# Kernel tuning notes

Measured on AMD Instinct MI355X. Metric: run time of the kernel, lower is better.

Reference implementation:

```python
import jax, jax.numpy as jnp
from jax import lax
import numpy as np

D_IN, D, H, W, POOL = 1280, 100, 20, 3, 9
K_SIG, X0 = 1.0, 0.0
EPS = 1e-5


def setup_inputs() -> dict:
    key = jax.random.key(0)
    ks = jax.random.split(key, 8)
    N1, N2 = 512, 512
    return {
        "x1": jax.random.normal(ks[0], (N1, D_IN), jnp.float32),
        "x2": jax.random.normal(ks[1], (N2, D_IN), jnp.float32),
        "W1": jax.random.normal(ks[2], (D, D_IN), jnp.float32) * 0.02,
        "b1": jnp.zeros((D,), jnp.float32),
        "W2": jax.random.normal(ks[3], (H, 2 * D), jnp.float32) * 0.05,
        "b2": jnp.zeros((H,), jnp.float32),
        "bn1_g": jnp.ones((H,), jnp.float32),
        "bn1_b": jnp.zeros((H,), jnp.float32),
        "conv_w": jax.random.normal(ks[4], (1, H, 2 * W + 1, 2 * W + 1), jnp.float32) * 0.05,
        "conv_b": jnp.zeros((1,), jnp.float32),
        "bn2_g": jnp.ones((1,), jnp.float32),
        "bn2_b": jnp.zeros((1,), jnp.float32),
        "gamma": jnp.zeros((1,), jnp.float32),
    }


def reference(x1, x2, W1, b1, W2, b2, bn1_g, bn1_b, conv_w, conv_b, bn2_g, bn2_b, gamma):
    N1, N2 = x1.shape[0], x2.shape[0]
    # fc1 projection (relu1/dropout1 are defined but unused in the original forward)
    a = (x1 @ W1.T + b1)[None]          # [1, N1, D]
    c = (x2 @ W1.T + b2 * 0 + b1)[None] if False else (x2 @ W1.T + b1)[None]  # [1, N2, D]
    # broadcast pairwise |diff| and product -> [1, N1, N2, 2D]
    diff = jnp.abs(a[:, :, None, :] - c[:, None, :, :])
    mul = a[:, :, None, :] * c[:, None, :, :]
    m = jnp.concatenate([diff, mul], axis=-1).reshape(-1, 2 * D)  # [N1*N2, 2D]
    # fc2
    m = m @ W2.T + b2                    # [N1*N2, H]
    # BatchNorm1d in training mode: batch statistics, biased variance
    mu = m.mean(axis=0)
    var = m.var(axis=0)
    m = (m - mu) * lax.rsqrt(var + EPS) * bn1_g + bn1_b
    m = jax.nn.relu(m)
    m = m.reshape(1, N1, N2, H).transpose(0, 3, 1, 2)  # NCHW [1, H, N1, N2]
    # 7x7 conv, padding=W
    C = lax.conv_general_dilated(m, conv_w, (1, 1), [(W, W), (W, W)])
    C = C + conv_b.reshape(1, -1, 1, 1)
    # BatchNorm2d (training mode, biased variance over N,H,W per channel)
    mu2 = C.mean(axis=(0, 2, 3), keepdims=True)
    var2 = C.var(axis=(0, 2, 3), keepdims=True)
    C = (C - mu2) * lax.rsqrt(var2 + EPS) * bn2_g.reshape(1, -1, 1, 1) + bn2_b.reshape(1, -1, 1, 1)
    C = jax.nn.sigmoid(C)
    # MaxPool2d(9, padding=4): stride = kernel, -inf padding
    p = POOL // 2
    B = lax.reduce_window(C, -jnp.inf, lax.max, (1, 1, POOL, POOL), (1, 1, POOL, POOL),
                          [(0, 0), (0, 0), (p, p), (p, p)])
    # mean / unbiased std over dims (1, 2) keepdim
    mean = B.mean(axis=(1, 2), keepdims=True)
    std = jnp.sqrt(B.var(axis=(1, 2), keepdims=True, ddof=1) + EPS)
    Q = jax.nn.relu(B - mean - gamma.reshape(()) * std)
    phat = Q.sum() / (jnp.sign(Q).sum() + 1.0)
    phat = jnp.clip(jax.nn.sigmoid(K_SIG * (phat - X0)), 0.0, 1.0)
    return phat, C
```

## Files before the change

### kernel.cpp

```cpp
#include <hip/hip_runtime.h>
#include <hip/hip_bf16.h>
#include <math.h>

#define N1 512
#define N2 512
#define DIN 1280
#define DD 100
#define HH 20
#define NPIX (N1*N2)
#define PB 57

typedef short bf16x8 __attribute__((ext_vector_type(8)));
typedef float f32x4 __attribute__((ext_vector_type(4)));

static constexpr size_t WS_PP    = 0;
static constexpr size_t WS_W1T   = 409600;
static constexpr size_t WS_W2B   = 537600;
static constexpr size_t WS_M     = 541696;
static constexpr size_t WS_PART  = WS_M + 5242880;
static constexpr size_t WS_CRAW  = WS_PART + 1310720;
static constexpr size_t WS_STATS = WS_CRAW + 262144;
static constexpr size_t WS_B     = WS_STATS + 64;

__global__ __launch_bounds__(256) void kP(const float* __restrict__ W1,
                                          const float* __restrict__ W2,
                                          float* __restrict__ w1t,
                                          unsigned short* __restrict__ w2b,
                                          float* __restrict__ stats) {
  const int tid = threadIdx.x;
  if (blockIdx.x >= 160) {
    int idx = (blockIdx.x - 160) * 256 + tid;
    if (blockIdx.x == 160 && tid < 64) stats[tid] = 0.0f;
    if (idx < 224 * 32) {
      int k = idx >> 5, n = idx & 31;
      float v = (n < HH && k < 200) ? W2[n * 200 + k] : 0.0f;
      __hip_bfloat16 b = __float2bfloat16(v);
      w2b[idx] = *reinterpret_cast<unsigned short*>(&b);
    }
    return;
  }
  __shared__ float sT[32][33];
  const int bx = blockIdx.x % 40, by = blockIdx.x / 40;
  const int tx = tid & 31, ty = tid >> 5;
#pragma unroll
  for (int e = 0; e < 4; ++e) {
    int h = by * 32 + ty + e * 8, k = bx * 32 + tx;
    sT[ty + e * 8][tx] = (h < DD) ? W1[(size_t)h * DIN + k] : 0.0f;
  }
  __syncthreads();
#pragma unroll
  for (int e = 0; e < 4; ++e) {
    int k = bx * 32 + ty + e * 8, h = by * 32 + tx;
    if (h < DD) w1t[(size_t)k * DD + h] = sT[tx][ty + e * 8];
  }
}

__global__ __launch_bounds__(256) void kA(const float* __restrict__ x1,
                                          const float* __restrict__ x2,
                                          const float* __restrict__ w1t,
                                          float* __restrict__ pp) {
  const int tid = threadIdx.x;
  const int w  = __builtin_amdgcn_readfirstlane(tid >> 6);
  const int rp = w >> 1, hh = w & 1;
  const int h = hh * 64 + (tid & 63);
  if (h >= DD) return;
  const int kq = blockIdx.x & 3;
  const int r0 = (blockIdx.x >> 2) * 4 + rp * 2;
  const float* xb = (r0 < N1) ? (x1 + (size_t)r0 * DIN) : (x2 + (size_t)(r0 - N1) * DIN);
  const float* xr0 = xb + kq * 320;
  const float* xr1 = xb + DIN + kq * 320;
  const float* w1p = w1t + (size_t)kq * 320 * DD + h;
  float a00 = 0.f, a01 = 0.f, a10 = 0.f, a11 = 0.f;
#pragma unroll 8
  for (int k = 0; k < 320; k += 2) {
    float wA = w1p[(size_t)k * DD];
    float wB = w1p[(size_t)(k + 1) * DD];
    a00 = fmaf(wA, xr0[k], a00); a01 = fmaf(wB, xr0[k + 1], a01);
    a10 = fmaf(wA, xr1[k], a10); a11 = fmaf(wB, xr1[k + 1], a11);
  }
  pp[(size_t)kq * 102400 + (size_t)r0 * DD + h] = a00 + a01;
  pp[(size_t)kq * 102400 + (size_t)(r0 + 1) * DD + h] = a10 + a11;
}

__global__ __launch_bounds__(256, 2) void kB(const float* __restrict__ pp,
                                             const float* __restrict__ b1,
                                             const unsigned short* __restrict__ w2b,
                                             float* __restrict__ m,
                                             float* __restrict__ stats) {
  __shared__ float sA[8][132];
  __shared__ float sC[64][132];
  __shared__ float wred[4][40];
  const int tid = threadIdx.x;
  const int bi = blockIdx.x >> 3, bj = blockIdx.x & 7;
  for (int idx = tid; idx < 72 * 33; idx += 256) {
    int r = idx / 33, d4 = idx % 33;
    float4 v = {0.f, 0.f, 0.f, 0.f};
    if (d4 < 25) {
      size_t row = (r < 8) ? (size_t)(bi * 8 + r) : (size_t)(N1 + bj * 64 + (r - 8));
      const float* base = pp + row * DD;
      float4 a0 = ((const float4*)base)[d4];
      float4 a1 = ((const float4*)(base + 102400))[d4];
      float4 a2 = ((const float4*)(base + 204800))[d4];
      float4 a3 = ((const float4*)(base + 307200))[d4];
      float4 bb = ((const float4*)b1)[d4];
      v.x = a0.x + a1.x + a2.x + a3.x + bb.x;
      v.y = a0.y + a1.y + a2.y + a3.y + bb.y;
      v.z = a0.z + a1.z + a2.z + a3.z + bb.z;
      v.w = a0.w + a1.w + a2.w + a3.w + bb.w;
    }
    if (r < 8) *(float4*)&sA[r][4 * d4] = v;
    else       *(float4*)&sC[r - 8][4 * d4] = v;
  }
  __syncthreads();
  const int w = tid >> 6, lane = tid & 63;
  const int ln = lane & 15, q = lane >> 4;
  const int jj = w * 16 + ln;
  bf16x8 af[7][2];
#pragma unroll
  for (int ks = 0; ks < 7; ++ks)
#pragma unroll
    for (int t = 0; t < 2; ++t) {
      bf16x8 v;
#pragma unroll
      for (int e = 0; e < 8; ++e)
        v[e] = (short)w2b[(ks * 32 + q * 8 + e) * 32 + ln + 16 * t];
      af[ks][t] = v;
    }
  int dOf[14];
  bool isP[14];
  float4 cH[14];
#pragma unroll
  for (int hx = 0; hx < 14; ++hx) {
    int kk = (hx >> 1) * 32 + q * 8 + (hx & 1) * 4;
    isP[hx] = kk >= 100;
    dOf[hx] = isP[hx] ? kk - 100 : kk;
    cH[hx] = *(const float4*)&sC[jj][dOf[hx]];
  }
  float st_s[8], st_q[8];
#pragma unroll
  for (int r = 0; r < 8; ++r) { st_s[r] = 0.f; st_q[r] = 0.f; }
  const int gj = bj * 64 + jj;
#pragma unroll 1
  for (int ii = 0; ii < 8; ++ii) {
    bf16x8 bf[7];
#pragma unroll
    for (int ks = 0; ks < 7; ++ks) {
      float4 a0 = *(const float4*)&sA[ii][dOf[2 * ks]];
      float4 a1 = *(const float4*)&sA[ii][dOf[2 * ks + 1]];
      float4 c0 = cH[2 * ks], c1 = cH[2 * ks + 1];
      float f0 = isP[2*ks]   ? a0.x * c0.x : fabsf(a0.x - c0.x);
      float f1 = isP[2*ks]   ? a0.y * c0.y : fabsf(a0.y - c0.y);
      float f2 = isP[2*ks]   ? a0.z * c0.z : fabsf(a0.z - c0.z);
      float f3 = isP[2*ks]   ? a0.w * c0.w : fabsf(a0.w - c0.w);
      float f4 = isP[2*ks+1] ? a1.x * c1.x : fabsf(a1.x - c1.x);
      float f5 = isP[2*ks+1] ? a1.y * c1.y : fabsf(a1.y - c1.y);
      float f6 = isP[2*ks+1] ? a1.z * c1.z : fabsf(a1.z - c1.z);
      float f7 = isP[2*ks+1] ? a1.w * c1.w : fabsf(a1.w - c1.w);
      union { bf16x8 v; __hip_bfloat162 h2[4]; } u;
      u.h2[0] = __float22bfloat162_rn(make_float2(f0, f1));
      u.h2[1] = __float22bfloat162_rn(make_float2(f2, f3));
      u.h2[2] = __float22bfloat162_rn(make_float2(f4, f5));
      u.h2[3] = __float22bfloat162_rn(make_float2(f6, f7));
      bf[ks] = u.v;
    }
    f32x4 acc0 = {0.f, 0.f, 0.f, 0.f}, acc1 = {0.f, 0.f, 0.f, 0.f};
#pragma unroll
    for (int ks = 0; ks < 7; ++ks) {
      acc0 = __builtin_amdgcn_mfma_f32_16x16x32_bf16(af[ks][0], bf[ks], acc0, 0, 0, 0);
      acc1 = __builtin_amdgcn_mfma_f32_16x16x32_bf16(af[ks][1], bf[ks], acc1, 0, 0, 0);
    }
    const size_t pix = (size_t)(bi * 8 + ii) * N2 + gj;
#pragma unroll
    for (int r = 0; r < 4; ++r) {
      m[(size_t)(4 * q + r) * NPIX + pix] = acc0[r];
      st_s[r] += acc0[r];
      st_q[r] += acc0[r] * acc0[r];
    }
    if (q == 0) {
#pragma unroll
      for (int r = 0; r < 4; ++r)
        m[(size_t)(16 + r) * NPIX + pix] = acc1[r];
    }
#pragma unroll
    for (int r = 0; r < 4; ++r) {
      st_s[4 + r] += acc1[r];
      st_q[4 + r] += acc1[r] * acc1[r];
    }
  }
#pragma unroll
  for (int r = 0; r < 8; ++r) {
#pragma unroll
    for (int off = 1; off < 16; off <<= 1) {
      st_s[r] += __shfl_xor(st_s[r], off);
      st_q[r] += __shfl_xor(st_q[r], off);
    }
  }
  if (ln == 0) {
#pragma unroll
    for (int r = 0; r < 4; ++r) {
      wred[w][4 * q + r]      = st_s[r];
      wred[w][20 + 4 * q + r] = st_q[r];
    }
    if (q == 0) {
#pragma unroll
      for (int r = 0; r < 4; ++r) {
        wred[w][16 + r] = st_s[4 + r];
        wred[w][36 + r] = st_q[4 + r];
      }
    }
  }
  __syncthreads();
  if (tid < 40)
    atomicAdd(&stats[tid], wred[0][tid] + wred[1][tid] + wred[2][tid] + wred[3][tid]);
}

__global__ __launch_bounds__(128, 2) void kD(const float* __restrict__ m,
                                             const float* __restrict__ bn1g,
                                             const float* __restrict__ bn1b,
                                             const float* __restrict__ cw,
                                             const float* __restrict__ stats,
                                             float* __restrict__ part) {
  __shared__ float sIn[4][38][42];
  __shared__ float sSc[4], sSh[4];
  const int tid = threadIdx.x;
  const int cs = blockIdx.y;
  if (tid < 4) {
    int ch = cs * 4 + tid;
    float s = stats[ch], q = stats[HH + ch];
    float mu = s * (1.0f / NPIX);
    float var = q * (1.0f / NPIX) - mu * mu;
    float g = bn1g[ch] / sqrtf(var + 1e-5f);
    sSc[tid] = g;
    sSh[tid] = bn1b[ch] - mu * g;
  }
  __syncthreads();
  const int by = (blockIdx.x >> 4) * 32, bx = (blockIdx.x & 15) * 32;
  for (int idx = tid; idx < 4 * 38 * 20; idx += 128) {
    int ch4 = idx / 760, rem = idx % 760;
    int r = rem / 20, c2 = rem % 20;
    int gy = by + r - 3, gx = bx + 2 * c2 - 4;
    float2 v = {0.f, 0.f};
    if (gy >= 0 && gy < N1 && gx >= 0 && gx < N2) {
      const float* mp = m + (size_t)(cs * 4 + ch4) * NPIX;
      float2 raw = *(const float2*)&mp[(size_t)gy * N2 + gx];
      float sc = sSc[ch4], sh = sSh[ch4];
      v.x = fmaxf(fmaf(raw.x, sc, sh), 0.0f);
      v.y = fmaxf(fmaf(raw.y, sc, sh), 0.0f);
    }
    *(float2*)&sIn[ch4][r][2 * c2] = v;
  }
  __syncthreads();
  const int ty = tid >> 4, tx = tid & 15;
  float acc[4][2];
#pragma unroll
  for (int o = 0; o < 4; ++o) { acc[o][0] = 0.f; acc[o][1] = 0.f; }
#pragma unroll 1
  for (int ch4 = 0; ch4 < 4; ++ch4) {
    const float* wch = cw + (cs * 4 + ch4) * 49;
#pragma unroll
    for (int wr = 0; wr < 10; ++wr) {
      float2 row[5];
#pragma unroll
      for (int qq = 0; qq < 5; ++qq)
        row[qq] = *(const float2*)&sIn[ch4][4 * ty + wr][2 * tx + 2 * qq];
#pragma unroll
      for (int o = 0; o < 4; ++o) {
        if (o > wr || wr - o > 6) continue;
        const int ky = wr - o;
#pragma unroll
        for (int kx = 0; kx < 7; ++kx) {
          float wt = wch[ky * 7 + kx];
          const int j0 = kx + 1, j1 = kx + 2;
          float e0 = (j0 & 1) ? row[j0 >> 1].y : row[j0 >> 1].x;
          float e1 = (j1 & 1) ? row[j1 >> 1].y : row[j1 >> 1].x;
          acc[o][0] = fmaf(e0, wt, acc[o][0]);
          acc[o][1] = fmaf(e1, wt, acc[o][1]);
        }
      }
    }
  }
  float* dst = part + (size_t)cs * NPIX;
  const int ox = bx + 2 * tx;
#pragma unroll
  for (int o = 0; o < 4; ++o) {
    const int oy = by + 4 * ty + o;
    float2 r0 = {acc[o][0], acc[o][1]};
    *(float2*)&dst[(size_t)oy * N2 + ox] = r0;
  }
}

__global__ __launch_bounds__(256) void kE1(const float* __restrict__ part,
                                           float* __restrict__ stats,
                                           float* __restrict__ Craw) {
  __shared__ float wred[4][2];
  const int i = blockIdx.x * 256 + threadIdx.x;
  float s5 = part[i] + part[NPIX + i] + part[2 * NPIX + i] + part[3 * NPIX + i] + part[4 * NPIX + i];
  Craw[i] = s5;
  float s = s5, q = s5 * s5;
  const int lane = threadIdx.x & 63, wv = threadIdx.x >> 6;
#pragma unroll
  for (int off = 32; off; off >>= 1) {
    s += __shfl_xor(s, off);
    q += __shfl_xor(q, off);
  }
  if (lane == 0) { wred[wv][0] = s; wred[wv][1] = q; }
  __syncthreads();
  if (threadIdx.x < 2) {
    float v = wred[0][threadIdx.x] + wred[1][threadIdx.x] + wred[2][threadIdx.x] + wred[3][threadIdx.x];
    atomicAdd(&stats[2 * HH + threadIdx.x], v);
  }
}

__global__ __launch_bounds__(256) void kE2M(const float* __restrict__ Craw,
                                            const float* __restrict__ stats,
                                            const float* __restrict__ bn2g,
                                            const float* __restrict__ bn2b,
                                            float* __restrict__ Cout,
                                            float* __restrict__ B) {
  const int w = blockIdx.x * 4 + (threadIdx.x >> 6);
  const int lane = threadIdx.x & 63;
  float s = stats[2 * HH], q = stats[2 * HH + 1];
  float mu = s * (1.0f / NPIX);
  float var = q * (1.0f / NPIX) - mu * mu;
  float g = bn2g[0] / sqrtf(var + 1e-5f);
  float b = bn2b[0] - mu * g;
  if (w >= PB * PB) return;
  const int wy = w / PB, wx = w % PB;
  const int y0 = wy * 9 - 4, x0 = wx * 9 - 4;
  float mx = -1e30f;
  for (int e = lane; e < 144; e += 64) {
    int dy = e / 12, dx = e % 12;
    int y = y0 + dy, x = x0 + dx;
    bool inWin = (dy < 9) && (dx < 9);
    bool claim = (y >= 0) && (y < N1) && (x >= 0) && (x < N2) &&
                 (dy < 9 || wy == PB - 1) && (dx < 9 || wx == PB - 1);
    if (claim) {
      float z = Craw[(size_t)y * N2 + x] * g + b;
      float sg = 1.0f / (1.0f + expf(-z));
      Cout[(size_t)y * N2 + x] = sg;
      if (inWin) mx = fmaxf(mx, sg);
    }
  }
#pragma unroll
  for (int off = 32; off; off >>= 1) mx = fmaxf(mx, __shfl_xor(mx, off));
  if (lane == 0) B[w] = mx;
}

__global__ __launch_bounds__(1024) void kF(const float* __restrict__ B,
                                           const float* __restrict__ gamma,
                                           float* __restrict__ out0) {
  __shared__ float sB[PB * PB];
  __shared__ float cm[PB], cs[PB];
  __shared__ float r1[16], r2[16];
  const int tid = threadIdx.x;
  for (int i = tid; i < PB * PB; i += 1024) sB[i] = B[i];
  __syncthreads();
  if (tid < PB * 16) {
    int c = tid >> 4, g = tid & 15;
    float s = 0.0f;
    for (int h = g; h < PB; h += 16) s += sB[h * PB + c];
#pragma unroll
    for (int off = 1; off < 16; off <<= 1) s += __shfl_xor(s, off);
    float mean = s / (float)PB;
    float v = 0.0f;
    for (int h = g; h < PB; h += 16) { float d = sB[h * PB + c] - mean; v += d * d; }
#pragma unroll
    for (int off = 1; off < 16; off <<= 1) v += __shfl_xor(v, off);
    if (g == 0) {
      cm[c] = mean;
      cs[c] = sqrtf(v / (float)(PB - 1) + 1e-5f);
    }
  }
  __syncthreads();
  const float g = gamma[0];
  float sq = 0.0f, cnt = 0.0f;
  for (int i = tid; i < PB * PB; i += 1024) {
    int w = i % PB;
    float qv = sB[i] - cm[w] - g * cs[w];
    if (qv > 0.0f) { sq += qv; cnt += 1.0f; }
  }
#pragma unroll
  for (int off = 32; off; off >>= 1) {
    sq += __shfl_xor(sq, off);
    cnt += __shfl_xor(cnt, off);
  }
  if ((tid & 63) == 0) { r1[tid >> 6] = sq; r2[tid >> 6] = cnt; }
  __syncthreads();
  if (tid == 0) {
    float S = 0.f, Cn = 0.f;
#pragma unroll
    for (int e = 0; e < 16; ++e) { S += r1[e]; Cn += r2[e]; }
    float phat = S / (Cn + 1.0f);
    float sig = 1.0f / (1.0f + expf(-phat));
    out0[0] = fminf(fmaxf(sig, 0.0f), 1.0f);
  }
}

extern "C" void kernel_launch(void* const* d_in, const int* in_sizes, int n_in,
                              void* d_out, int out_size, void* d_ws, size_t ws_size,
                              hipStream_t stream) {
  const float* x1    = (const float*)d_in[0];
  const float* x2    = (const float*)d_in[1];
  const float* W1    = (const float*)d_in[2];
  const float* b1    = (const float*)d_in[3];
  const float* W2    = (const float*)d_in[4];
  const float* bn1g  = (const float*)d_in[6];
  const float* bn1b  = (const float*)d_in[7];
  const float* convw = (const float*)d_in[8];
  const float* bn2g  = (const float*)d_in[10];
  const float* bn2b  = (const float*)d_in[11];
  const float* gamma = (const float*)d_in[12];

  float* ws    = (float*)d_ws;
  float* pp    = ws + WS_PP;
  float* w1t   = ws + WS_W1T;
  unsigned short* w2b = (unsigned short*)(ws + WS_W2B);
  float* m     = ws + WS_M;
  float* part  = ws + WS_PART;
  float* Craw  = ws + WS_CRAW;
  float* stats = ws + WS_STATS;
  float* Bp    = ws + WS_B;
  float* out   = (float*)d_out;

  kP<<<188, 256, 0, stream>>>(W1, W2, w1t, w2b, stats);
  kA<<<1024, 256, 0, stream>>>(x1, x2, w1t, pp);
  kB<<<512, 256, 0, stream>>>(pp, b1, w2b, m, stats);
  kD<<<dim3(256, 5), 128, 0, stream>>>(m, bn1g, bn1b, convw, stats, part);
  kE1<<<1024, 256, 0, stream>>>(part, stats, Craw);
  kE2M<<<(PB * PB + 3) / 4, 256, 0, stream>>>(Craw, stats, bn2g, bn2b, out + 1, Bp);
  kF<<<1, 1024, 0, stream>>>(Bp, gamma, out);
}
```

Before: 95.30 us.

## Store fc2 activations as bf16 and retile the conv kernel

The fc2 output m (20 channels × 262144 pixels) is now written as bf16 instead of fp32, which halves the traffic of the write in kB and the read in kD. The conv kernel kD now uses 256 threads with 64×16 output tiles and vectorized ushort4 loads that convert bf16 back to float. The W2 conversion and stats zeroing move from kP into extra blocks of kA. BN1 statistics are still accumulated from the fp32 values, but the conv input now carries bf16 rounding error.

```diff
diff --git a/kernel.cpp b/kernel.cpp
--- a/kernel.cpp
+++ b/kernel.cpp
@@ -9,28 +9,56 @@
 #define HH 20
 #define NPIX (N1*N2)
 #define PB 57
+#define NWIN (PB*PB)
 
 typedef short bf16x8 __attribute__((ext_vector_type(8)));
 typedef float f32x4 __attribute__((ext_vector_type(4)));
+
+static __device__ __forceinline__ float bf16f(unsigned short u) {
+  union { unsigned int i; float f; } c;
+  c.i = ((unsigned int)u) << 16;
+  return c.f;
+}
 
 static constexpr size_t WS_PP    = 0;
 static constexpr size_t WS_W1T   = 409600;
 static constexpr size_t WS_W2B   = 537600;
 static constexpr size_t WS_M     = 541696;
-static constexpr size_t WS_PART  = WS_M + 5242880;
+static constexpr size_t WS_PART  = WS_M + 2621440;
 static constexpr size_t WS_CRAW  = WS_PART + 1310720;
 static constexpr size_t WS_STATS = WS_CRAW + 262144;
 static constexpr size_t WS_B     = WS_STATS + 64;
 
 __global__ __launch_bounds__(256) void kP(const float* __restrict__ W1,
+                                          float* __restrict__ w1t) {
+  const int tid = threadIdx.x;
+  __shared__ float sT[32][33];
+  const int bx = blockIdx.x % 40, by = blockIdx.x / 40;
+  const int tx = tid & 31, ty = tid >> 5;
+#pragma unroll
+  for (int e = 0; e < 4; ++e) {
+    int h = by * 32 + ty + e * 8, k = bx * 32 + tx;
+    sT[ty + e * 8][tx] = (h < DD) ? W1[(size_t)h * DIN + k] : 0.0f;
+  }
+  __syncthreads();
+#pragma unroll
+  for (int e = 0; e < 4; ++e) {
+    int k = bx * 32 + ty + e * 8, h = by * 32 + tx;
+    if (h < DD) w1t[(size_t)k * DD + h] = sT[tx][ty + e * 8];
+  }
+}
+
+__global__ __launch_bounds__(256) void kA(const float* __restrict__ x1,
+                                          const float* __restrict__ x2,
+                                          const float* __restrict__ w1t,
                                           const float* __restrict__ W2,
-                                          float* __restrict__ w1t,
+                                          float* __restrict__ pp,
                                           unsigned short* __restrict__ w2b,
                                           float* __restrict__ stats) {
   const int tid = threadIdx.x;
-  if (blockIdx.x >= 160) {
-    int idx = (blockIdx.x - 160) * 256 + tid;
-    if (blockIdx.x == 160 && tid < 64) stats[tid] = 0.0f;
+  if (blockIdx.x >= 1024) {
+    int idx = (blockIdx.x - 1024) * 256 + tid;
+    if (blockIdx.x == 1024 && tid < 64) stats[tid] = 0.0f;
     if (idx < 224 * 32) {
       int k = idx >> 5, n = idx & 31;
       float v = (n < HH && k < 200) ? W2[n * 200 + k] : 0.0f;
@@ -39,27 +67,6 @@
     }
     return;
   }
-  __shared__ float sT[32][33];
-  const int bx = blockIdx.x % 40, by = blockIdx.x / 40;
-  const int tx = tid & 31, ty = tid >> 5;
-#pragma unroll
-  for (int e = 0; e < 4; ++e) {
-    int h = by * 32 + ty + e * 8, k = bx * 32 + tx;
-    sT[ty + e * 8][tx] = (h < DD) ? W1[(size_t)h * DIN + k] : 0.0f;
-  }
-  __syncthreads();
-#pragma unroll
-  for (int e = 0; e < 4; ++e) {
-    int k = bx * 32 + ty + e * 8, h = by * 32 + tx;
-    if (h < DD) w1t[(size_t)k * DD + h] = sT[tx][ty + e * 8];
-  }
-}
-
-__global__ __launch_bounds__(256) void kA(const float* __restrict__ x1,
-                                          const float* __restrict__ x2,
-                                          const float* __restrict__ w1t,
-                                          float* __restrict__ pp) {
-  const int tid = threadIdx.x;
   const int w  = __builtin_amdgcn_readfirstlane(tid >> 6);
   const int rp = w >> 1, hh = w & 1;
   const int h = hh * 64 + (tid & 63);
@@ -85,7 +92,7 @@
 __global__ __launch_bounds__(256, 2) void kB(const float* __restrict__ pp,
                                              const float* __restrict__ b1,
                                              const unsigned short* __restrict__ w2b,
-                                             float* __restrict__ m,
+                                             unsigned short* __restrict__ m16,
                                              float* __restrict__ stats) {
   __shared__ float sA[8][132];
   __shared__ float sC[64][132];
@@ -172,14 +179,17 @@
     const size_t pix = (size_t)(bi * 8 + ii) * N2 + gj;
 #pragma unroll
     for (int r = 0; r < 4; ++r) {
-      m[(size_t)(4 * q + r) * NPIX + pix] = acc0[r];
+      __hip_bfloat16 hb = __float2bfloat16(acc0[r]);
+      m16[(size_t)(4 * q + r) * NPIX + pix] = *reinterpret_cast<unsigned short*>(&hb);
       st_s[r] += acc0[r];
       st_q[r] += acc0[r] * acc0[r];
     }
     if (q == 0) {
 #pragma unroll
-      for (int r = 0; r < 4; ++r)
-        m[(size_t)(16 + r) * NPIX + pix] = acc1[r];
+      for (int r = 0; r < 4; ++r) {
+        __hip_bfloat16 hb = __float2bfloat16(acc1[r]);
+        m16[(size_t)(16 + r) * NPIX + pix] = *reinterpret_cast<unsigned short*>(&hb);
+      }
     }
 #pragma unroll
     for (int r = 0; r < 4; ++r) {
@@ -214,13 +224,13 @@
     atomicAdd(&stats[tid], wred[0][tid] + wred[1][tid] + wred[2][tid] + wred[3][tid]);
 }
 
-__global__ __launch_bounds__(128, 2) void kD(const float* __restrict__ m,
-                                             const float* __restrict__ bn1g,
-                                             const float* __restrict__ bn1b,
-                                             const float* __restrict__ cw,
-                                             const float* __restrict__ stats,
-                                             float* __restrict__ part) {
-  __shared__ float sIn[4][38][42];
+__global__ __launch_bounds__(256) void kD(const unsigned short* __restrict__ m16,
+                                          const float* __restrict__ bn1g,
+                                          const float* __restrict__ bn1b,
+                                          const float* __restrict__ cw,
+                                          const float* __restrict__ stats,
+                                          float* __restrict__ part) {
+  __shared__ float sIn[4][22][74];
   __shared__ float sSc[4], sSh[4];
   const int tid = threadIdx.x;
   const int cs = blockIdx.y;
@@ -234,59 +244,66 @@
     sSh[tid] = bn1b[ch] - mu * g;
   }
   __syncthreads();
-  const int by = (blockIdx.x >> 4) * 32, bx = (blockIdx.x & 15) * 32;
-  for (int idx = tid; idx < 4 * 38 * 20; idx += 128) {
-    int ch4 = idx / 760, rem = idx % 760;
-    int r = rem / 20, c2 = rem % 20;
-    int gy = by + r - 3, gx = bx + 2 * c2 - 4;
-    float2 v = {0.f, 0.f};
-    if (gy >= 0 && gy < N1 && gx >= 0 && gx < N2) {
-      const float* mp = m + (size_t)(cs * 4 + ch4) * NPIX;
-      float2 raw = *(const float2*)&mp[(size_t)gy * N2 + gx];
-      float sc = sSc[ch4], sh = sSh[ch4];
-      v.x = fmaxf(fmaf(raw.x, sc, sh), 0.0f);
-      v.y = fmaxf(fmaf(raw.y, sc, sh), 0.0f);
-    }
-    *(float2*)&sIn[ch4][r][2 * c2] = v;
-  }
-  __syncthreads();
-  const int ty = tid >> 4, tx = tid & 15;
-  float acc[4][2];
-#pragma unroll
-  for (int o = 0; o < 4; ++o) { acc[o][0] = 0.f; acc[o][1] = 0.f; }
+  const int bx = (blockIdx.x & 7) * 64, by = (blockIdx.x >> 3) * 16;
+  for (int idx = tid; idx < 4 * 22 * 18; idx += 256) {
+    int ch4 = idx / (22 * 18), rem = idx % (22 * 18);
+    int r = rem / 18, p = rem % 18;
+    int gy = by + r - 3;
+    int gx0 = bx + 4 * p - 4;
+    float sc = sSc[ch4], sh = sSh[ch4];
+    float v[4] = {0.f, 0.f, 0.f, 0.f};
+    if (gy >= 0 && gy < N1) {
+      const unsigned short* mp = m16 + (size_t)(cs * 4 + ch4) * NPIX + (size_t)gy * N2;
+      if (gx0 >= 0 && gx0 + 3 < N2) {
+        ushort4 u = *(const ushort4*)&mp[gx0];
+        v[0] = fmaxf(fmaf(bf16f(u.x), sc, sh), 0.0f);
+        v[1] = fmaxf(fmaf(bf16f(u.y), sc, sh), 0.0f);
+        v[2] = fmaxf(fmaf(bf16f(u.z), sc, sh), 0.0f);
+        v[3] = fmaxf(fmaf(bf16f(u.w), sc, sh), 0.0f);
+      } else {
+#pragma unroll
+        for (int j = 0; j < 4; ++j) {
+          int gx = gx0 + j;
+          if (gx >= 0 && gx < N2)
+            v[j] = fmaxf(fmaf(bf16f(mp[gx]), sc, sh), 0.0f);
+        }
+      }
+    }
+    *(float4*)&sIn[ch4][r][4 * p] = make_float4(v[0], v[1], v[2], v[3]);
+  }
+  __syncthreads();
+  const int tx = tid & 31, ty = tid >> 5;
+  float acc00 = 0.f, acc01 = 0.f, acc10 = 0.f, acc11 = 0.f;
 #pragma unroll 1
   for (int ch4 = 0; ch4 < 4; ++ch4) {
     const float* wch = cw + (cs * 4 + ch4) * 49;
 #pragma unroll
-    for (int wr = 0; wr < 10; ++wr) {
-      float2 row[5];
+    for (int wr = 0; wr < 8; ++wr) {
+      float2 rowv[5];
 #pragma unroll
       for (int qq = 0; qq < 5; ++qq)
-        row[qq] = *(const float2*)&sIn[ch4][4 * ty + wr][2 * tx + 2 * qq];
-#pragma unroll
-      for (int o = 0; o < 4; ++o) {
-        if (o > wr || wr - o > 6) continue;
+        rowv[qq] = *(const float2*)&sIn[ch4][2 * ty + wr][2 * tx + 2 * qq];
+#pragma unroll
+      for (int o = 0; o < 2; ++o) {
+        if (wr - o < 0 || wr - o > 6) continue;
         const int ky = wr - o;
 #pragma unroll
         for (int kx = 0; kx < 7; ++kx) {
           float wt = wch[ky * 7 + kx];
           const int j0 = kx + 1, j1 = kx + 2;
-          float e0 = (j0 & 1) ? row[j0 >> 1].y : row[j0 >> 1].x;
-          float e1 = (j1 & 1) ? row[j1 >> 1].y : row[j1 >> 1].x;
-          acc[o][0] = fmaf(e0, wt, acc[o][0]);
-          acc[o][1] = fmaf(e1, wt, acc[o][1]);
+          float e0 = (j0 & 1) ? rowv[j0 >> 1].y : rowv[j0 >> 1].x;
+          float e1 = (j1 & 1) ? rowv[j1 >> 1].y : rowv[j1 >> 1].x;
+          if (o == 0) { acc00 = fmaf(e0, wt, acc00); acc01 = fmaf(e1, wt, acc01); }
+          else        { acc10 = fmaf(e0, wt, acc10); acc11 = fmaf(e1, wt, acc11); }
         }
       }
     }
   }
   float* dst = part + (size_t)cs * NPIX;
   const int ox = bx + 2 * tx;
-#pragma unroll
-  for (int o = 0; o < 4; ++o) {
-    const int oy = by + 4 * ty + o;
-    float2 r0 = {acc[o][0], acc[o][1]};
-    *(float2*)&dst[(size_t)oy * N2 + ox] = r0;
-  }
+  float2 r0 = {acc00, acc01}, r1 = {acc10, acc11};
+  *(float2*)&dst[(size_t)(by + 2 * ty) * N2 + ox] = r0;
+  *(float2*)&dst[(size_t)(by + 2 * ty + 1) * N2 + ox] = r1;
 }
 
 __global__ __launch_bounds__(256) void kE1(const float* __restrict__ part,
@@ -324,7 +341,7 @@
   float var = q * (1.0f / NPIX) - mu * mu;
   float g = bn2g[0] / sqrtf(var + 1e-5f);
   float b = bn2b[0] - mu * g;
-  if (w >= PB * PB) return;
+  if (w >= NWIN) return;
   const int wy = w / PB, wx = w % PB;
   const int y0 = wy * 9 - 4, x0 = wx * 9 - 4;
   float mx = -1e30f;
@@ -349,11 +366,11 @@
 __global__ __launch_bounds__(1024) void kF(const float* __restrict__ B,
                                            const float* __restrict__ gamma,
                                            float* __restrict__ out0) {
-  __shared__ float sB[PB * PB];
+  __shared__ float sB[NWIN];
   __shared__ float cm[PB], cs[PB];
   __shared__ float r1[16], r2[16];
   const int tid = threadIdx.x;
-  for (int i = tid; i < PB * PB; i += 1024) sB[i] = B[i];
+  for (int i = tid; i < NWIN; i += 1024) sB[i] = B[i];
   __syncthreads();
   if (tid < PB * 16) {
     int c = tid >> 4, g = tid & 15;
@@ -374,7 +391,7 @@
   __syncthreads();
   const float g = gamma[0];
   float sq = 0.0f, cnt = 0.0f;
-  for (int i = tid; i < PB * PB; i += 1024) {
+  for (int i = tid; i < NWIN; i += 1024) {
     int w = i % PB;
     float qv = sB[i] - cm[w] - g * cs[w];
     if (qv > 0.0f) { sq += qv; cnt += 1.0f; }
@@ -415,18 +432,18 @@
   float* pp    = ws + WS_PP;
   float* w1t   = ws + WS_W1T;
   unsigned short* w2b = (unsigned short*)(ws + WS_W2B);
-  float* m     = ws + WS_M;
+  unsigned short* m16 = (unsigned short*)(ws + WS_M);
   float* part  = ws + WS_PART;
   float* Craw  = ws + WS_CRAW;
   float* stats = ws + WS_STATS;
   float* Bp    = ws + WS_B;
   float* out   = (float*)d_out;
 
-  kP<<<188, 256, 0, stream>>>(W1, W2, w1t, w2b, stats);
-  kA<<<1024, 256, 0, stream>>>(x1, x2, w1t, pp);
-  kB<<<512, 256, 0, stream>>>(pp, b1, w2b, m, stats);
-  kD<<<dim3(256, 5), 128, 0, stream>>>(m, bn1g, bn1b, convw, stats, part);
+  kP<<<160, 256, 0, stream>>>(W1, w1t);
+  kA<<<1052, 256, 0, stream>>>(x1, x2, w1t, W2, pp, w2b, stats);
+  kB<<<512, 256, 0, stream>>>(pp, b1, w2b, m16, stats);
+  kD<<<dim3(256, 5), 256, 0, stream>>>(m16, bn1g, bn1b, convw, stats, part);
   kE1<<<1024, 256, 0, stream>>>(part, stats, Craw);
-  kE2M<<<(PB * PB + 3) / 4, 256, 0, stream>>>(Craw, stats, bn2g, bn2b, out + 1, Bp);
+  kE2M<<<(NWIN + 3) / 4, 256, 0, stream>>>(Craw, stats, bn2g, bn2b, out + 1, Bp);
   kF<<<1, 1024, 0, stream>>>(Bp, gamma, out);
 }
```

Result: faster. 89.81 us (-5.8%).
